# Optimization experiments

Measured on AMD Instinct MI355X. Metric: run time of the kernel, lower is better.

Reference implementation:

```python
import jax, jax.numpy as jnp
import numpy as np

N = 50000          # nodes
E = 1600000        # edges
F_IN = 128         # num_features
H = 256            # hidden_channels
ED = 64            # edge_dims
NL = 8             # num_layouts
NC = 10            # num_classes
NG = 64            # num graphs
NEG_SLOPE = 0.2


def _mkw(key, shape, fan_in):
    return jax.random.normal(key, shape, dtype=jnp.float32) * (1.0 / np.sqrt(fan_in))


def setup_inputs() -> dict:
    key = jax.random.key(0)
    ks = jax.random.split(key, 32)
    x = jax.random.normal(ks[0], (N, F_IN), dtype=jnp.float32)
    edge_index = jax.random.randint(ks[1], (2, E), 0, N)
    edge_attr_raw = jax.random.normal(ks[2], (E, NL), dtype=jnp.float32)
    batch = jnp.sort(jax.random.randint(ks[3], (N,), 0, NG))
    # PermutationInvariantNet params
    pm_w1 = _mkw(ks[4], (NL, H), NL); pm_b1 = jnp.zeros((H,), jnp.float32)
    pm_w2 = _mkw(ks[5], (H, ED), H); pm_b2 = jnp.zeros((ED,), jnp.float32)
    pm_ws = _mkw(ks[6], (ED + 3, ED), ED + 3); pm_bs = jnp.zeros((ED,), jnp.float32)
    # GATv2Conv layer 1 (in F_IN -> H, 1 head): lin_l (src), lin_r (dst), lin_edge, att
    g1_wl = _mkw(ks[7], (F_IN, H), F_IN); g1_bl = jnp.zeros((H,), jnp.float32)
    g1_wr = _mkw(ks[8], (F_IN, H), F_IN)
    g1_we = _mkw(ks[9], (ED, H), ED)
    g1_att = _mkw(ks[10], (H,), H)
    g1_bo = jnp.zeros((H,), jnp.float32)
    # GATv2Conv layer 2 (H -> H)
    g2_wl = _mkw(ks[11], (H, H), H); g2_bl = jnp.zeros((H,), jnp.float32)
    g2_wr = _mkw(ks[12], (H, H), H)
    g2_we = _mkw(ks[13], (ED, H), ED)
    g2_att = _mkw(ks[14], (H,), H)
    g2_bo = jnp.zeros((H,), jnp.float32)
    # edge update linears
    w2 = _mkw(ks[15], (2 * H, ED), 2 * H); b2 = jnp.zeros((ED,), jnp.float32)
    w3 = _mkw(ks[16], (2 * ED, ED), 2 * ED); b3 = jnp.zeros((ED,), jnp.float32)
    # final classifier
    w1 = _mkw(ks[17], (H, NC), H); b1 = jnp.zeros((NC,), jnp.float32)
    return dict(x=x, edge_index=edge_index, edge_attr_raw=edge_attr_raw, batch=batch,
                pm_w1=pm_w1, pm_b1=pm_b1, pm_w2=pm_w2, pm_b2=pm_b2, pm_ws=pm_ws, pm_bs=pm_bs,
                g1_wl=g1_wl, g1_bl=g1_bl, g1_wr=g1_wr, g1_we=g1_we, g1_att=g1_att, g1_bo=g1_bo,
                g2_wl=g2_wl, g2_bl=g2_bl, g2_wr=g2_wr, g2_we=g2_we, g2_att=g2_att, g2_bo=g2_bo,
                w2=w2, b2=b2, w3=w3, b3=b3, w1=w1, b1=b1)


def perm_invariant_net(x, w1, b1, w2, b2, ws, bs):
    xs = jnp.sort(x, axis=1)  # [E, NL]
    f = jax.nn.relu(xs @ w1 + b1) @ w2 + b2  # [E, ED]
    x_max = xs[:, -1]
    x_min = xs[:, 0]
    x_range = x_max - x_min
    x_std = jnp.std(xs, axis=1, ddof=1)
    comb = jnp.concatenate([f, x_range[:, None], x_std[:, None], x_max[:, None]], axis=1)
    return jax.nn.relu(comb @ ws + bs)


def gatv2_conv(x_src, edge_index, edge_attr, wl, bl, wr, we, att, bo):
    # single head GATv2 with edge features
    src, dst = edge_index[0], edge_index[1]
    xl = x_src @ wl + bl         # source transform [N,H]
    xr = x_src @ wr              # target transform [N,H]
    e = edge_attr @ we           # [E,H]
    s = xl[src] + xr[dst] + e    # [E,H]
    logits = jax.nn.leaky_relu(s, NEG_SLOPE) @ att  # [E]
    # softmax over incoming edges of each dst node
    m = jnp.full((x_src.shape[0],), -jnp.inf, jnp.float32).at[dst].max(logits)
    ex = jnp.exp(logits - m[dst])
    denom = jax.ops.segment_sum(ex, dst, num_segments=x_src.shape[0])
    alpha = ex / denom[dst]
    msg = xl[src] * alpha[:, None]  # [E,H]
    out = jax.ops.segment_sum(msg, dst, num_segments=x_src.shape[0])
    return out + bo


def reference(x, edge_index, edge_attr_raw, batch,
              pm_w1, pm_b1, pm_w2, pm_b2, pm_ws, pm_bs,
              g1_wl, g1_bl, g1_wr, g1_we, g1_att, g1_bo,
              g2_wl, g2_bl, g2_wr, g2_we, g2_att, g2_bo,
              w2, b2, w3, b3, w1, b1):
    edge_attr = perm_invariant_net(edge_attr_raw, pm_w1, pm_b1, pm_w2, pm_b2, pm_ws, pm_bs)
    h = gatv2_conv(x, edge_index, edge_attr, g1_wl, g1_bl, g1_wr, g1_we, g1_att, g1_bo)
    # edge update: gather endpoints, linear, concat, linear
    xi = h[edge_index[0]]
    xj = h[edge_index[1]]
    message = jnp.concatenate([xi, xj], axis=1) @ w2 + b2
    edge_attr = jnp.concatenate([edge_attr, message], axis=1) @ w3 + b3
    h = jax.nn.relu(h)
    h = gatv2_conv(h, edge_index, edge_attr, g2_wl, g2_bl, g2_wr, g2_we, g2_att, g2_bo)
    h = jax.nn.relu(h)
    pooled = jax.ops.segment_sum(h, batch, num_segments=NG)  # [NG,H]
    logits = pooled @ w1 + b1
    return jax.nn.log_softmax(logits, axis=1)
```

## Files before the change

kernel.cpp:

```cpp
#include <hip/hip_runtime.h>
#include <cstdint>
#include <cstddef>

#define N_NODES 50000
#define NE      1600000
#define FIN     128
#define HDIM    256
#define EDIM    64
#define NGR     64
#define NCLS    10

using short8 = __attribute__((ext_vector_type(8))) short;
using f32x4  = __attribute__((ext_vector_type(4))) float;

__device__ __forceinline__ float b2f(unsigned short u) {
  union { uint32_t i; float f; } v; v.i = ((uint32_t)u) << 16; return v.f;
}
__device__ __forceinline__ unsigned short f2b(float f) {
  union { float f; uint32_t i; } v; v.f = f;
  uint32_t r = v.i + 0x7fff + ((v.i >> 16) & 1);
  return (unsigned short)(r >> 16);
}

__global__ void k_count(const int* __restrict__ dst, int* __restrict__ cnt) {
  int e = blockIdx.x * 256 + threadIdx.x;
  if (e < NE) atomicAdd(&cnt[dst[e]], 1);
}

__global__ __launch_bounds__(1024) void k_scan(int* __restrict__ cnt, int* __restrict__ rp) {
  __shared__ int s[1024];
  __shared__ int base_s;
  int t = threadIdx.x;
  if (t == 0) { base_s = 0; rp[0] = 0; }
  __syncthreads();
  for (int c0 = 0; c0 < N_NODES; c0 += 1024) {
    int i = c0 + t;
    int v = (i < N_NODES) ? cnt[i] : 0;
    s[t] = v;
    __syncthreads();
    for (int off = 1; off < 1024; off <<= 1) {
      int add = (t >= off) ? s[t - off] : 0;
      __syncthreads();
      s[t] += add;
      __syncthreads();
    }
    int incl = s[t];
    int base = base_s;
    if (i < N_NODES) {
      int excl = base + incl - v;
      cnt[i] = excl;
      rp[i]  = excl;
      if (i == N_NODES - 1) rp[N_NODES] = base + incl;
    }
    __syncthreads();
    if (t == 1023) base_s = base + incl;
    __syncthreads();
  }
}

__global__ void k_scatter(const int* __restrict__ src, const int* __restrict__ dst,
                          int* __restrict__ cur, int* __restrict__ ssrc,
                          int* __restrict__ epos) {
  int e = blockIdx.x * 256 + threadIdx.x;
  if (e < NE) {
    int d = dst[e];
    int pos = atomicAdd(&cur[d], 1);
    ssrc[pos] = src[e];
    epos[e] = pos;
  }
}

__global__ __launch_bounds__(256) void k_pre1(const float* __restrict__ w3,
    const float* __restrict__ g2we, float* __restrict__ M, float* __restrict__ Wa) {
  int idx = blockIdx.x * 256 + threadIdx.x;
  int which = idx >> 14;
  int k = (idx >> 8) & 63, d = idx & 255;
  const float* wrow = w3 + (size_t)(which ? k : (64 + k)) * 64;
  float a = 0.f;
#pragma unroll 8
  for (int j = 0; j < 64; j++) a = fmaf(wrow[j], g2we[j * 256 + d], a);
  (which ? Wa : M)[k * 256 + d] = a;
}

__global__ __launch_bounds__(256) void k_pre2(const float* __restrict__ w2,
    const float* __restrict__ b2, const float* __restrict__ b3,
    const float* __restrict__ M, const float* __restrict__ g2we,
    float* __restrict__ Ths, float* __restrict__ Thd, float* __restrict__ bias2) {
  int idx = blockIdx.x * 256 + threadIdx.x;
  if (idx < 65536) {
    int k = idx >> 8, d = idx & 255;
    float a = 0.f;
#pragma unroll 8
    for (int j = 0; j < 64; j++) a = fmaf(w2[(size_t)k * 64 + j], M[j * 256 + d], a);
    Ths[(size_t)k * 256 + d] = a;
  } else if (idx < 131072) {
    int k = (idx - 65536) >> 8, d = idx & 255;
    float a = 0.f;
#pragma unroll 8
    for (int j = 0; j < 64; j++) a = fmaf(w2[(size_t)(256 + k) * 64 + j], M[j * 256 + d], a);
    Thd[(size_t)k * 256 + d] = a;
  } else if (idx < 131328) {
    int d = idx - 131072;
    float a = 0.f;
#pragma unroll 8
    for (int j = 0; j < 64; j++) {
      a = fmaf(b2[j], M[j * 256 + d], a);
      a = fmaf(b3[j], g2we[j * 256 + d], a);
    }
    bias2[d] = a;
  }
}

__global__ __launch_bounds__(256) void k_prew(const float* __restrict__ W,
                                              unsigned short* __restrict__ WT) {
  int idx = blockIdx.x * 256 + threadIdx.x;
  int n = idx >> 6, k = idx & 63;
  WT[idx] = f2b(W[k * 256 + n]);
}

__global__ __launch_bounds__(256) void k_perm(const float* __restrict__ raw,
    const float* __restrict__ pw1, const float* __restrict__ pb1,
    const float* __restrict__ pw2, const float* __restrict__ pb2,
    const float* __restrict__ pws, const float* __restrict__ pbs,
    uint8_t* __restrict__ Q, float* __restrict__ SC) {
  int e = blockIdx.x * 256 + threadIdx.x;
  const float4* rp4 = reinterpret_cast<const float4*>(raw + (size_t)e * 8);
  float4 v0 = rp4[0], v1 = rp4[1];
  float x0 = v0.x, x1 = v0.y, x2 = v0.z, x3 = v0.w;
  float x4 = v1.x, x5 = v1.y, x6 = v1.z, x7 = v1.w;
#define CE(a,b) { float lo_ = fminf(a,b), hi_ = fmaxf(a,b); a = lo_; b = hi_; }
  CE(x0,x1) CE(x2,x3) CE(x4,x5) CE(x6,x7)
  CE(x0,x2) CE(x1,x3) CE(x4,x6) CE(x5,x7)
  CE(x1,x2) CE(x5,x6) CE(x0,x4) CE(x3,x7)
  CE(x1,x5) CE(x2,x6)
  CE(x1,x4) CE(x3,x6)
  CE(x2,x4) CE(x3,x5)
  CE(x3,x4)
#undef CE
  float xs[8] = {x0,x1,x2,x3,x4,x5,x6,x7};
  float sum = x0+x1+x2+x3+x4+x5+x6+x7;
  float mean = sum * 0.125f;
  float var = 0.f;
#pragma unroll
  for (int i = 0; i < 8; i++) { float d = xs[i] - mean; var = fmaf(d, d, var); }
  float sd  = sqrtf(var * (1.f / 7.f));
  float rng = x7 - x0;
  float mx  = x7;

  float f[64];
#pragma unroll
  for (int o = 0; o < 64; o++) f[o] = pb2[o];
#pragma unroll 2
  for (int j = 0; j < 256; j++) {
    float h = pb1[j];
#pragma unroll
    for (int i = 0; i < 8; i++) h = fmaf(xs[i], pw1[i * 256 + j], h);
    h = fmaxf(h, 0.f);
#pragma unroll
    for (int o = 0; o < 64; o++) f[o] = fmaf(h, pw2[j * 64 + o], f[o]);
  }
  float g[64];
#pragma unroll
  for (int o = 0; o < 64; o++)
    g[o] = pbs[o] + rng * pws[64 * 64 + o] + sd * pws[65 * 64 + o] + mx * pws[66 * 64 + o];
#pragma unroll
  for (int k = 0; k < 64; k++) {
    float fk = f[k];
#pragma unroll
    for (int o = 0; o < 64; o++) g[o] = fmaf(fk, pws[k * 64 + o], g[o]);
  }
  float mrow = 0.f;
#pragma unroll
  for (int o = 0; o < 64; o++) { g[o] = fmaxf(g[o], 0.f); mrow = fmaxf(mrow, g[o]); }
  float inv = (mrow > 0.f) ? (255.f / mrow) : 0.f;
  SC[e] = mrow * (1.f / 255.f);
  uint32_t pk[16];
#pragma unroll
  for (int w = 0; w < 16; w++) {
    uint32_t q0 = (uint32_t)(g[4*w+0] * inv + 0.5f);
    uint32_t q1 = (uint32_t)(g[4*w+1] * inv + 0.5f);
    uint32_t q2 = (uint32_t)(g[4*w+2] * inv + 0.5f);
    uint32_t q3 = (uint32_t)(g[4*w+3] * inv + 0.5f);
    pk[w] = q0 | (q1 << 8) | (q2 << 16) | (q3 << 24);
  }
  uint4* qp = reinterpret_cast<uint4*>(Q + (size_t)e * 64);
#pragma unroll
  for (int w = 0; w < 4; w++) {
    uint4 v; v.x = pk[4*w]; v.y = pk[4*w+1]; v.z = pk[4*w+2]; v.w = pk[4*w+3];
    qp[w] = v;
  }
}

template<bool BIAS>
__global__ __launch_bounds__(256) void k_gemm_x(const float* __restrict__ A,
    const float* __restrict__ W, const float* __restrict__ bias,
    unsigned short* __restrict__ out, int Mrows) {
  __shared__ float As[32][68];
  __shared__ float Bs[32][64];
  int t = threadIdx.x;
  int m0 = blockIdx.x * 64, n0 = blockIdx.y * 64;
  int tm = t & 15, tn = t >> 4;
  float acc[4][4] = {};
  for (int k0 = 0; k0 < FIN; k0 += 32) {
    {
      int e = t >> 2, kk = (t & 3) * 8;
      int gm = m0 + e;
      float va[8];
      if (gm < Mrows) {
        const float* ap = A + (size_t)gm * FIN + k0 + kk;
        float4 a0 = *reinterpret_cast<const float4*>(ap);
        float4 a1 = *reinterpret_cast<const float4*>(ap + 4);
        va[0]=a0.x; va[1]=a0.y; va[2]=a0.z; va[3]=a0.w;
        va[4]=a1.x; va[5]=a1.y; va[6]=a1.z; va[7]=a1.w;
      } else {
#pragma unroll
        for (int q = 0; q < 8; q++) va[q] = 0.f;
      }
#pragma unroll
      for (int q = 0; q < 8; q++) As[kk + q][e] = va[q];
    }
    {
      int r = t >> 3, c = (t & 7) * 8;
      const float* wp = W + (size_t)(k0 + r) * 256 + n0 + c;
      *reinterpret_cast<float4*>(&Bs[r][c])     = *reinterpret_cast<const float4*>(wp);
      *reinterpret_cast<float4*>(&Bs[r][c + 4]) = *reinterpret_cast<const float4*>(wp + 4);
    }
    __syncthreads();
#pragma unroll
    for (int k = 0; k < 32; k++) {
      float4 a4 = *reinterpret_cast<const float4*>(&As[k][tm * 4]);
      float4 b4 = *reinterpret_cast<const float4*>(&Bs[k][tn * 4]);
      float av[4] = {a4.x, a4.y, a4.z, a4.w};
      float bv[4] = {b4.x, b4.y, b4.z, b4.w};
#pragma unroll
      for (int i = 0; i < 4; i++)
#pragma unroll
        for (int j = 0; j < 4; j++)
          acc[i][j] = fmaf(av[i], bv[j], acc[i][j]);
    }
    __syncthreads();
  }
  float bv4[4] = {0.f, 0.f, 0.f, 0.f};
  if (BIAS) {
#pragma unroll
    for (int j = 0; j < 4; j++) bv4[j] = bias[n0 + tn * 4 + j];
  }
#pragma unroll
  for (int i = 0; i < 4; i++) {
    int gm = m0 + tm * 4 + i;
    if (gm < Mrows) {
      ushort4 o;
      o.x = f2b(acc[i][0] + bv4[0]); o.y = f2b(acc[i][1] + bv4[1]);
      o.z = f2b(acc[i][2] + bv4[2]); o.w = f2b(acc[i][3] + bv4[3]);
      *reinterpret_cast<ushort4*>(out + (size_t)gm * 256 + n0 + tn * 4) = o;
    }
  }
}

template<bool W2P, bool BIAS>
__global__ __launch_bounds__(256) void k_gemm_h(const unsigned short* __restrict__ H,
    const float* __restrict__ W1, const float* __restrict__ W2,
    const float* __restrict__ bias, unsigned short* __restrict__ out, int Mrows) {
  __shared__ float As[32][68];
  __shared__ float Bs[32][64];
  int t = threadIdx.x;
  int m0 = blockIdx.x * 64, n0 = blockIdx.y * 64;
  int tm = t & 15, tn = t >> 4;
  float acc[4][4] = {};
  const int passes = W2P ? 2 : 1;
  for (int ps = 0; ps < passes; ps++) {
    const float* W = ps ? W2 : W1;
    for (int k0 = 0; k0 < HDIM; k0 += 32) {
      {
        int e = t >> 2, kk = (t & 3) * 8;
        int gm = m0 + e;
        float va[8];
        if (gm < Mrows) {
          uint4 hv = *reinterpret_cast<const uint4*>(H + (size_t)gm * 256 + k0 + kk);
          uint32_t wd[4] = {hv.x, hv.y, hv.z, hv.w};
#pragma unroll
          for (int q = 0; q < 4; q++) {
            va[2*q]   = b2f((unsigned short)(wd[q] & 0xffff));
            va[2*q+1] = b2f((unsigned short)(wd[q] >> 16));
          }
        } else {
#pragma unroll
          for (int q = 0; q < 8; q++) va[q] = 0.f;
        }
#pragma unroll
        for (int q = 0; q < 8; q++) {
          float v = va[q];
          if (ps == 0) v = fmaxf(v, 0.f);
          As[kk + q][e] = v;
        }
      }
      {
        int r = t >> 3, c = (t & 7) * 8;
        const float* wp = W + (size_t)(k0 + r) * 256 + n0 + c;
        *reinterpret_cast<float4*>(&Bs[r][c])     = *reinterpret_cast<const float4*>(wp);
        *reinterpret_cast<float4*>(&Bs[r][c + 4]) = *reinterpret_cast<const float4*>(wp + 4);
      }
      __syncthreads();
#pragma unroll
      for (int k = 0; k < 32; k++) {
        float4 a4 = *reinterpret_cast<const float4*>(&As[k][tm * 4]);
        float4 b4 = *reinterpret_cast<const float4*>(&Bs[k][tn * 4]);
        float av[4] = {a4.x, a4.y, a4.z, a4.w};
        float bv[4] = {b4.x, b4.y, b4.z, b4.w};
#pragma unroll
        for (int i = 0; i < 4; i++)
#pragma unroll
          for (int j = 0; j < 4; j++)
            acc[i][j] = fmaf(av[i], bv[j], acc[i][j]);
      }
      __syncthreads();
    }
  }
  float bv4[4] = {0.f, 0.f, 0.f, 0.f};
  if (BIAS) {
#pragma unroll
    for (int j = 0; j < 4; j++) bv4[j] = bias[n0 + tn * 4 + j];
  }
#pragma unroll
  for (int i = 0; i < 4; i++) {
    int gm = m0 + tm * 4 + i;
    if (gm < Mrows) {
      ushort4 o;
      o.x = f2b(acc[i][0] + bv4[0]); o.y = f2b(acc[i][1] + bv4[1]);
      o.z = f2b(acc[i][2] + bv4[2]); o.w = f2b(acc[i][3] + bv4[3]);
      *reinterpret_cast<ushort4*>(out + (size_t)gm * 256 + n0 + tn * 4) = o;
    }
  }
}

template<bool EBIAS>
__global__ __launch_bounds__(256) void k_elogit(
    const uint8_t* __restrict__ Q, const float* __restrict__ SC,
    const int* __restrict__ src, const int* __restrict__ dst,
    const int* __restrict__ epos,
    const unsigned short* __restrict__ xl, const unsigned short* __restrict__ xr,
    const unsigned short* __restrict__ WT, const float* __restrict__ att,
    const float* __restrict__ ebias, float* __restrict__ lg) {
  __shared__ int   s_src[64], s_dst[64], s_pos[64];
  __shared__ float att_s[256];
  __shared__ float eb_s[256];
  int t = threadIdx.x;
  int e0 = blockIdx.x * 64;
  if (t < 64) { s_src[t] = src[e0 + t]; s_dst[t] = dst[e0 + t]; s_pos[t] = epos[e0 + t]; }
  att_s[t] = att[t];
  if (EBIAS) eb_s[t] = ebias[t];
  __syncthreads();

  int w = t >> 6, l = t & 63;
  int la = l & 15, kg = l >> 4;
  int ebase = w * 16;

  const uint8_t* qrow = Q + (size_t)(e0 + ebase + la) * 64 + kg * 8;
  uint2 qa = *reinterpret_cast<const uint2*>(qrow);
  uint2 qb = *reinterpret_cast<const uint2*>(qrow + 32);
  float sc = SC[e0 + ebase + la];
  short8 a0, a1;
#pragma unroll
  for (int j = 0; j < 4; j++) {
    a0[j]     = (short)f2b((float)((qa.x >> (8 * j)) & 0xff) * sc);
    a0[4 + j] = (short)f2b((float)((qa.y >> (8 * j)) & 0xff) * sc);
    a1[j]     = (short)f2b((float)((qb.x >> (8 * j)) & 0xff) * sc);
    a1[4 + j] = (short)f2b((float)((qb.y >> (8 * j)) & 0xff) * sc);
  }

  f32x4 acc[16];
#pragma unroll
  for (int nt = 0; nt < 16; nt++) acc[nt] = (f32x4){0.f, 0.f, 0.f, 0.f};
#pragma unroll
  for (int nt = 0; nt < 16; nt++) {
    const unsigned short* wtp = WT + (size_t)(nt * 16 + la) * 64 + kg * 8;
    short8 b0 = *reinterpret_cast<const short8*>(wtp);
    short8 b1 = *reinterpret_cast<const short8*>(wtp + 32);
    acc[nt] = __builtin_amdgcn_mfma_f32_16x16x32_bf16(a0, b0, acc[nt], 0, 0, 0);
    acc[nt] = __builtin_amdgcn_mfma_f32_16x16x32_bf16(a1, b1, acc[nt], 0, 0, 0);
  }

  float p[4] = {0.f, 0.f, 0.f, 0.f};
#pragma unroll
  for (int nt = 0; nt < 16; nt++) {
    int n = nt * 16 + la;
    float attn = att_s[n];
    float ebn = EBIAS ? eb_s[n] : 0.f;
#pragma unroll
    for (int r = 0; r < 4; r++) {
      int e = ebase + kg * 4 + r;
      float xlv = b2f(xl[(size_t)s_src[e] * 256 + n]);
      float xrv = b2f(xr[(size_t)s_dst[e] * 256 + n]);
      float sv = acc[nt][r] + xlv + xrv + ebn;
      sv = (sv > 0.f) ? sv : 0.2f * sv;
      p[r] = fmaf(sv, attn, p[r]);
    }
  }
#pragma unroll
  for (int r = 0; r < 4; r++) {
    float v = p[r];
    v += __shfl_xor(v, 1);
    v += __shfl_xor(v, 2);
    v += __shfl_xor(v, 4);
    v += __shfl_xor(v, 8);
    p[r] = v;
  }
  if (la == 0) {
#pragma unroll
    for (int r = 0; r < 4; r++) {
      int e = ebase + kg * 4 + r;
      lg[s_pos[e]] = p[r];
    }
  }
}

template<bool POOL>
__global__ __launch_bounds__(256) void k_agg(const int* __restrict__ rp,
    const int* __restrict__ ssrc, const float* __restrict__ lg,
    const unsigned short* __restrict__ xl, const float* __restrict__ bo,
    const int* __restrict__ batch,
    unsigned short* __restrict__ out_b, float* __restrict__ out_pool) {
  int n = blockIdx.x, t = threadIdx.x;
  int beg = rp[n], deg = rp[n + 1] - beg;
  __shared__ float ws_[256];
  __shared__ int   ss_[256];
  __shared__ float rbuf[256];
  float lm = -3.4e38f;
  for (int i = t; i < deg; i += 256) lm = fmaxf(lm, lg[beg + i]);
  rbuf[t] = lm; __syncthreads();
  for (int s = 128; s > 0; s >>= 1) { if (t < s) rbuf[t] = fmaxf(rbuf[t], rbuf[t + s]); __syncthreads(); }
  float m = rbuf[0];
  __syncthreads();
  float acc = 0.f, dpart = 0.f;
  for (int c0 = 0; c0 < deg; c0 += 256) {
    int i = c0 + t;
    float w = 0.f; int sidx = 0;
    if (i < deg) { w = expf(lg[beg + i] - m); sidx = ssrc[beg + i]; dpart += w; }
    ws_[t] = w; ss_[t] = sidx;
    __syncthreads();
    int lim = min(256, deg - c0);
    for (int j = 0; j < lim; j++)
      acc = fmaf(ws_[j], b2f(xl[(size_t)ss_[j] * 256 + t]), acc);
    __syncthreads();
  }
  rbuf[t] = dpart; __syncthreads();
  for (int s = 128; s > 0; s >>= 1) { if (t < s) rbuf[t] += rbuf[t + s]; __syncthreads(); }
  float denom = rbuf[0];
  float val = ((denom > 0.f) ? acc / denom : 0.f) + bo[t];
  if (POOL) {
    val = fmaxf(val, 0.f);
    atomicAdd(&out_pool[(size_t)batch[n] * 256 + t], val);
  } else {
    out_b[(size_t)n * 256 + t] = f2b(val);
  }
}

__global__ __launch_bounds__(256) void k_final(const float* __restrict__ pooled,
    const float* __restrict__ fw, const float* __restrict__ fb,
    float* __restrict__ out) {
  __shared__ float ps[256];
  __shared__ float ls[NCLS];
  __shared__ float lse_s;
  int g = blockIdx.x, t = threadIdx.x;
  ps[t] = pooled[(size_t)g * 256 + t];
  __syncthreads();
  if (t < NCLS) {
    float a = fb[t];
    for (int k = 0; k < 256; k++) a = fmaf(ps[k], fw[k * NCLS + t], a);
    ls[t] = a;
  }
  __syncthreads();
  if (t == 0) {
    float mxv = ls[0];
    for (int c = 1; c < NCLS; c++) mxv = fmaxf(mxv, ls[c]);
    float se = 0.f;
    for (int c = 0; c < NCLS; c++) se += expf(ls[c] - mxv);
    lse_s = mxv + logf(se);
  }
  __syncthreads();
  if (t < NCLS) out[g * NCLS + t] = ls[t] - lse_s;
}

extern "C" void kernel_launch(void* const* d_in, const int* in_sizes, int n_in,
                              void* d_out, int out_size, void* d_ws, size_t ws_size,
                              hipStream_t stream) {
  (void)in_sizes; (void)n_in; (void)out_size; (void)ws_size;
  const float* x     = (const float*)d_in[0];
  const int*   ei    = (const int*)d_in[1];
  const int*   src   = ei;
  const int*   dst   = ei + NE;
  const float* raw   = (const float*)d_in[2];
  const int*   batch = (const int*)d_in[3];
  const float* pm_w1 = (const float*)d_in[4];
  const float* pm_b1 = (const float*)d_in[5];
  const float* pm_w2 = (const float*)d_in[6];
  const float* pm_b2 = (const float*)d_in[7];
  const float* pm_ws = (const float*)d_in[8];
  const float* pm_bs = (const float*)d_in[9];
  const float* g1_wl = (const float*)d_in[10];
  const float* g1_bl = (const float*)d_in[11];
  const float* g1_wr = (const float*)d_in[12];
  const float* g1_we = (const float*)d_in[13];
  const float* g1_att= (const float*)d_in[14];
  const float* g1_bo = (const float*)d_in[15];
  const float* g2_wl = (const float*)d_in[16];
  const float* g2_bl = (const float*)d_in[17];
  const float* g2_wr = (const float*)d_in[18];
  const float* g2_we = (const float*)d_in[19];
  const float* g2_att= (const float*)d_in[20];
  const float* g2_bo = (const float*)d_in[21];
  const float* w2    = (const float*)d_in[22];
  const float* b2    = (const float*)d_in[23];
  const float* w3    = (const float*)d_in[24];
  const float* b3    = (const float*)d_in[25];
  const float* w1    = (const float*)d_in[26];
  const float* b1    = (const float*)d_in[27];

  char* wp = (char*)d_ws;
  auto alloc = [&](size_t bytes) -> void* {
    void* p = (void*)wp;
    wp += (bytes + 255) & ~(size_t)255;
    return p;
  };
  uint8_t* Q    = (uint8_t*)alloc((size_t)NE * 64);
  float*   SCq  = (float*)alloc((size_t)NE * 4);
  unsigned short* NB0 = (unsigned short*)alloc((size_t)N_NODES * 256 * 2);
  unsigned short* NB1 = (unsigned short*)alloc((size_t)N_NODES * 256 * 2);
  unsigned short* NB2 = (unsigned short*)alloc((size_t)N_NODES * 256 * 2);
  unsigned short* NB3 = (unsigned short*)alloc((size_t)N_NODES * 256 * 2);
  float* LG   = (float*)alloc((size_t)NE * 4);
  int*   EPOS = (int*)alloc((size_t)NE * 4);
  int*   SSRC = (int*)alloc((size_t)NE * 4);
  int*   RP   = (int*)alloc((size_t)(N_NODES + 1) * 4);
  int*   CUR  = (int*)alloc((size_t)N_NODES * 4);
  float* POOL = (float*)alloc((size_t)NGR * 256 * 4);
  float* Mm   = (float*)alloc((size_t)64 * 256 * 4);
  float* Wa   = (float*)alloc((size_t)64 * 256 * 4);
  float* Ths  = (float*)alloc((size_t)256 * 256 * 4);
  float* Thd  = (float*)alloc((size_t)256 * 256 * 4);
  float* B2V  = (float*)alloc((size_t)256 * 4);
  unsigned short* WT1 = (unsigned short*)alloc((size_t)256 * 64 * 2);
  unsigned short* WT2 = (unsigned short*)alloc((size_t)256 * 64 * 2);

  hipMemsetAsync(CUR, 0, (size_t)N_NODES * 4, stream);
  hipMemsetAsync(POOL, 0, (size_t)NGR * 256 * 4, stream);

  k_count  <<<NE / 256, 256, 0, stream>>>(dst, CUR);
  k_scan   <<<1, 1024, 0, stream>>>(CUR, RP);
  k_scatter<<<NE / 256, 256, 0, stream>>>(src, dst, CUR, SSRC, EPOS);

  k_pre1<<<128, 256, 0, stream>>>(w3, g2_we, Mm, Wa);
  k_pre2<<<513, 256, 0, stream>>>(w2, b2, b3, Mm, g2_we, Ths, Thd, B2V);
  k_prew<<<64, 256, 0, stream>>>(g1_we, WT1);
  k_prew<<<64, 256, 0, stream>>>(Wa, WT2);

  k_perm<<<NE / 256, 256, 0, stream>>>(raw, pm_w1, pm_b1, pm_w2, pm_b2, pm_ws, pm_bs, Q, SCq);

  dim3 gg((N_NODES + 63) / 64, 4);
  k_gemm_x<true ><<<gg, 256, 0, stream>>>(x, g1_wl, g1_bl, NB0, N_NODES);
  k_gemm_x<false><<<gg, 256, 0, stream>>>(x, g1_wr, nullptr, NB1, N_NODES);
  k_elogit<false><<<NE / 64, 256, 0, stream>>>(Q, SCq, src, dst, EPOS, NB0, NB1,
                                               WT1, g1_att, nullptr, LG);
  k_agg<false><<<N_NODES, 256, 0, stream>>>(RP, SSRC, LG, NB0, g1_bo, batch, NB2, nullptr);

  k_gemm_h<false, true ><<<gg, 256, 0, stream>>>(NB2, g2_wl, nullptr, g2_bl, NB3, N_NODES);
  k_gemm_h<true,  true ><<<gg, 256, 0, stream>>>(NB2, g2_wl, Ths, g2_bl, NB0, N_NODES);
  k_gemm_h<true,  false><<<gg, 256, 0, stream>>>(NB2, g2_wr, Thd, nullptr, NB1, N_NODES);

  k_elogit<true><<<NE / 64, 256, 0, stream>>>(Q, SCq, src, dst, EPOS, NB0, NB1,
                                              WT2, g2_att, B2V, LG);
  k_agg<true><<<N_NODES, 256, 0, stream>>>(RP, SSRC, LG, NB3, g2_bo, batch, nullptr, POOL);

  k_final<<<NGR, 256, 0, stream>>>(POOL, w1, b1, (float*)d_out);
}
```

Measured before the change: 3.405 ms.

## Move permutation-invariant MLP to bf16 MFMA with wave-cooperative edge tiles

Rewrites the per-edge perm-net kernel so each wave handles 16 edges. The two 256->64 and 64->64 matmuls run on bf16 MFMA instructions instead of scalar FMAs per thread, and pre-transposed bf16 weights come from a new prep kernel. Intermediate features and quantized outputs are staged through shared memory, and the row max is computed with cross-lane shuffles. This removes a very FMA-heavy, register-heavy scalar loop, but the hidden activations and features are now rounded to bf16, which reduces precision.

Result: slower. 3.513 ms (+3.2%).

```diff
diff --git a/kernel.cpp b/kernel.cpp
--- a/kernel.cpp
+++ b/kernel.cpp
@@ -118,13 +118,36 @@
   WT[idx] = f2b(W[k * 256 + n]);
 }
 
+__global__ __launch_bounds__(256) void k_prewp(const float* __restrict__ w2m,
+    const float* __restrict__ wsm, unsigned short* __restrict__ w2T,
+    unsigned short* __restrict__ wsT) {
+  int idx = blockIdx.x * 256 + threadIdx.x;
+  if (idx < 16384) {
+    int f = idx >> 8, h = idx & 255;
+    w2T[idx] = f2b(w2m[h * 64 + f]);
+  } else if (idx < 20480) {
+    int i2 = idx - 16384;
+    int g = i2 >> 6, fd = i2 & 63;
+    wsT[i2] = f2b(wsm[fd * 64 + g]);
+  }
+}
+
 __global__ __launch_bounds__(256) void k_perm(const float* __restrict__ raw,
     const float* __restrict__ pw1, const float* __restrict__ pb1,
-    const float* __restrict__ pw2, const float* __restrict__ pb2,
-    const float* __restrict__ pws, const float* __restrict__ pbs,
+    const unsigned short* __restrict__ pw2T, const float* __restrict__ pb2,
+    const unsigned short* __restrict__ pwsT, const float* __restrict__ pws,
+    const float* __restrict__ pbs,
     uint8_t* __restrict__ Q, float* __restrict__ SC) {
-  int e = blockIdx.x * 256 + threadIdx.x;
-  const float4* rp4 = reinterpret_cast<const float4*>(raw + (size_t)e * 8);
+  __shared__ unsigned short fbuf[4][16][72];
+  __shared__ uint8_t qbuf[4][16][80];
+  __shared__ float4 stat_s[4][16];
+  int t = threadIdx.x;
+  int w = t >> 6, l = t & 63;
+  int la = l & 15, kg = l >> 4;
+  int e0w = blockIdx.x * 64 + w * 16;
+  int eg = e0w + la;
+
+  const float4* rp4 = reinterpret_cast<const float4*>(raw + (size_t)eg * 8);
   float4 v0 = rp4[0], v1 = rp4[1];
   float x0 = v0.x, x1 = v0.y, x2 = v0.z, x3 = v0.w;
   float x4 = v1.x, x5 = v1.y, x6 = v1.z, x7 = v1.w;
@@ -146,49 +169,96 @@
   float sd  = sqrtf(var * (1.f / 7.f));
   float rng = x7 - x0;
   float mx  = x7;
-
-  float f[64];
-#pragma unroll
-  for (int o = 0; o < 64; o++) f[o] = pb2[o];
-#pragma unroll 2
-  for (int j = 0; j < 256; j++) {
-    float h = pb1[j];
-#pragma unroll
-    for (int i = 0; i < 8; i++) h = fmaf(xs[i], pw1[i * 256 + j], h);
-    h = fmaxf(h, 0.f);
-#pragma unroll
-    for (int o = 0; o < 64; o++) f[o] = fmaf(h, pw2[j * 64 + o], f[o]);
-  }
-  float g[64];
-#pragma unroll
-  for (int o = 0; o < 64; o++)
-    g[o] = pbs[o] + rng * pws[64 * 64 + o] + sd * pws[65 * 64 + o] + mx * pws[66 * 64 + o];
-#pragma unroll
-  for (int k = 0; k < 64; k++) {
-    float fk = f[k];
-#pragma unroll
-    for (int o = 0; o < 64; o++) g[o] = fmaf(fk, pws[k * 64 + o], g[o]);
-  }
-  float mrow = 0.f;
-#pragma unroll
-  for (int o = 0; o < 64; o++) { g[o] = fmaxf(g[o], 0.f); mrow = fmaxf(mrow, g[o]); }
-  float inv = (mrow > 0.f) ? (255.f / mrow) : 0.f;
-  SC[e] = mrow * (1.f / 255.f);
-  uint32_t pk[16];
-#pragma unroll
-  for (int w = 0; w < 16; w++) {
-    uint32_t q0 = (uint32_t)(g[4*w+0] * inv + 0.5f);
-    uint32_t q1 = (uint32_t)(g[4*w+1] * inv + 0.5f);
-    uint32_t q2 = (uint32_t)(g[4*w+2] * inv + 0.5f);
-    uint32_t q3 = (uint32_t)(g[4*w+3] * inv + 0.5f);
-    pk[w] = q0 | (q1 << 8) | (q2 << 16) | (q3 << 24);
-  }
-  uint4* qp = reinterpret_cast<uint4*>(Q + (size_t)e * 64);
-#pragma unroll
-  for (int w = 0; w < 4; w++) {
-    uint4 v; v.x = pk[4*w]; v.y = pk[4*w+1]; v.z = pk[4*w+2]; v.w = pk[4*w+3];
-    qp[w] = v;
-  }
+  if (kg == 0) stat_s[w][la] = make_float4(rng, sd, mx, 0.f);
+
+  short8 hfr[8];
+#pragma unroll
+  for (int kt = 0; kt < 8; kt++) {
+    int d0 = kt * 32 + kg * 8;
+    float4 b1a = *reinterpret_cast<const float4*>(pb1 + d0);
+    float4 b1b = *reinterpret_cast<const float4*>(pb1 + d0 + 4);
+    float hv[8] = {b1a.x, b1a.y, b1a.z, b1a.w, b1b.x, b1b.y, b1b.z, b1b.w};
+#pragma unroll
+    for (int j = 0; j < 8; j++) {
+      float4 wa = *reinterpret_cast<const float4*>(pw1 + j * 256 + d0);
+      float4 wb = *reinterpret_cast<const float4*>(pw1 + j * 256 + d0 + 4);
+      float xj = xs[j];
+      hv[0] = fmaf(xj, wa.x, hv[0]); hv[1] = fmaf(xj, wa.y, hv[1]);
+      hv[2] = fmaf(xj, wa.z, hv[2]); hv[3] = fmaf(xj, wa.w, hv[3]);
+      hv[4] = fmaf(xj, wb.x, hv[4]); hv[5] = fmaf(xj, wb.y, hv[5]);
+      hv[6] = fmaf(xj, wb.z, hv[6]); hv[7] = fmaf(xj, wb.w, hv[7]);
+    }
+#pragma unroll
+    for (int i = 0; i < 8; i++) hfr[kt][i] = (short)f2b(fmaxf(hv[i], 0.f));
+  }
+
+#pragma unroll
+  for (int rt = 0; rt < 4; rt++) {
+    f32x4 acc = {0.f, 0.f, 0.f, 0.f};
+#pragma unroll
+    for (int kt = 0; kt < 8; kt++) {
+      short8 af = *reinterpret_cast<const short8*>(
+          pw2T + (size_t)(rt * 16 + la) * 256 + kt * 32 + kg * 8);
+      acc = __builtin_amdgcn_mfma_f32_16x16x32_bf16(af, hfr[kt], acc, 0, 0, 0);
+    }
+    int fd0 = rt * 16 + kg * 4;
+    ushort4 fw4;
+    fw4.x = f2b(acc[0] + pb2[fd0 + 0]);
+    fw4.y = f2b(acc[1] + pb2[fd0 + 1]);
+    fw4.z = f2b(acc[2] + pb2[fd0 + 2]);
+    fw4.w = f2b(acc[3] + pb2[fd0 + 3]);
+    *reinterpret_cast<ushort4*>(&fbuf[w][la][fd0]) = fw4;
+  }
+  __syncthreads();
+
+  short8 af0 = *reinterpret_cast<const short8*>(&fbuf[w][la][kg * 8]);
+  short8 af1 = *reinterpret_cast<const short8*>(&fbuf[w][la][32 + kg * 8]);
+  f32x4 gacc[4];
+#pragma unroll
+  for (int nt = 0; nt < 4; nt++) {
+    const unsigned short* bp = pwsT + (size_t)(nt * 16 + la) * 64;
+    short8 b0 = *reinterpret_cast<const short8*>(bp + kg * 8);
+    short8 b1v = *reinterpret_cast<const short8*>(bp + 32 + kg * 8);
+    f32x4 a = {0.f, 0.f, 0.f, 0.f};
+    a = __builtin_amdgcn_mfma_f32_16x16x32_bf16(af0, b0, a, 0, 0, 0);
+    a = __builtin_amdgcn_mfma_f32_16x16x32_bf16(af1, b1v, a, 0, 0, 0);
+    gacc[nt] = a;
+  }
+
+  float4 st[4];
+#pragma unroll
+  for (int r = 0; r < 4; r++) st[r] = stat_s[w][kg * 4 + r];
+  float gv[4][4];
+#pragma unroll
+  for (int nt = 0; nt < 4; nt++) {
+    int gd = nt * 16 + la;
+    float w64 = pws[64 * 64 + gd];
+    float w65 = pws[65 * 64 + gd];
+    float w66 = pws[66 * 64 + gd];
+    float bsv = pbs[gd];
+#pragma unroll
+    for (int r = 0; r < 4; r++) {
+      float val = gacc[nt][r] + bsv + st[r].x * w64 + st[r].y * w65 + st[r].z * w66;
+      gv[r][nt] = fmaxf(val, 0.f);
+    }
+  }
+#pragma unroll
+  for (int r = 0; r < 4; r++) {
+    float m = fmaxf(fmaxf(gv[r][0], gv[r][1]), fmaxf(gv[r][2], gv[r][3]));
+    m = fmaxf(m, __shfl_xor(m, 1));
+    m = fmaxf(m, __shfl_xor(m, 2));
+    m = fmaxf(m, __shfl_xor(m, 4));
+    m = fmaxf(m, __shfl_xor(m, 8));
+    if (la == 0) SC[e0w + kg * 4 + r] = m * (1.f / 255.f);
+    float inv = (m > 0.f) ? (255.f / m) : 0.f;
+#pragma unroll
+    for (int nt = 0; nt < 4; nt++)
+      qbuf[w][kg * 4 + r][nt * 16 + la] = (uint8_t)(gv[r][nt] * inv + 0.5f);
+  }
+  __syncthreads();
+
+  uint4 qv = *reinterpret_cast<const uint4*>(&qbuf[w][la][kg * 16]);
+  *reinterpret_cast<uint4*>(Q + (size_t)(e0w + la) * 64 + kg * 16) = qv;
 }
 
 template<bool BIAS>
@@ -541,6 +611,8 @@
   float* B2V  = (float*)alloc((size_t)256 * 4);
   unsigned short* WT1 = (unsigned short*)alloc((size_t)256 * 64 * 2);
   unsigned short* WT2 = (unsigned short*)alloc((size_t)256 * 64 * 2);
+  unsigned short* PW2T = (unsigned short*)alloc((size_t)64 * 256 * 2);
+  unsigned short* PWST = (unsigned short*)alloc((size_t)64 * 64 * 2);
 
   hipMemsetAsync(CUR, 0, (size_t)N_NODES * 4, stream);
   hipMemsetAsync(POOL, 0, (size_t)NGR * 256 * 4, stream);
@@ -553,8 +625,10 @@
   k_pre2<<<513, 256, 0, stream>>>(w2, b2, b3, Mm, g2_we, Ths, Thd, B2V);
   k_prew<<<64, 256, 0, stream>>>(g1_we, WT1);
   k_prew<<<64, 256, 0, stream>>>(Wa, WT2);
-
-  k_perm<<<NE / 256, 256, 0, stream>>>(raw, pm_w1, pm_b1, pm_w2, pm_b2, pm_ws, pm_bs, Q, SCq);
+  k_prewp<<<80, 256, 0, stream>>>(pm_w2, pm_ws, PW2T, PWST);
+
+  k_perm<<<NE / 64, 256, 0, stream>>>(raw, pm_w1, pm_b1, PW2T, pm_b2, PWST,
+                                      pm_ws, pm_bs, Q, SCq);
 
   dim3 gg((N_NODES + 63) / 64, 4);
   k_gemm_x<true ><<<gg, 256, 0, stream>>>(x, g1_wl, g1_bl, NB0, N_NODES);
```
